# Optimization experiments

Hardware: AMD Instinct MI355X
Metric: run time of the kernel (lower is better)

The kernel has to match this reference:

```python
import jax, jax.numpy as jnp
import numpy as np

EPS = 1e-8


def setup_inputs() -> dict:
    key = jax.random.key(0)
    k1, k2 = jax.random.split(key)
    a = jax.random.normal(k1, (1, 256, 128, 128), dtype=jnp.float32)
    b = jax.random.normal(k2, (1, 256, 128, 128), dtype=jnp.float32)
    return {"a": a, "b": b}


def reference(a, b):
    # a: [n, c, h, w] rendered feats; b: [n, c, h2, w2] style feats (n == 1)
    n, c, h, w = a.shape
    a_flat = a.reshape(n, c, -1)            # [n, c, hw]
    b_flat = b.reshape(n, c, -1)            # [n, c, h2w2]

    # argmin_cos_distance: channel-wise L2 normalize, cosine distance, argmin
    b_norm = jnp.sqrt((b_flat * b_flat).sum(1, keepdims=True) + EPS)
    b_n = b_flat / (b_norm + EPS)
    a_norm = jnp.sqrt((a_flat * a_flat).sum(1, keepdims=True) + EPS)
    a_n = a_flat / (a_norm + EPS)
    d_mat = 1.0 - jnp.einsum('ncp,ncq->npq', a_n, b_n)   # [n, hw, h2w2]
    z_best = jnp.argmin(d_mat, axis=2)                    # [n, hw]

    # nn_feat_replace: gather matched (unnormalized) style features
    idx = jnp.broadcast_to(z_best[:, None, :], b_flat.shape)
    target = jnp.take_along_axis(b_flat, idx, axis=2).reshape(n, c, h, w)

    # cos_loss(a, target): cosine distance over channel dim, mean over pixels
    an = jnp.sqrt((a * a).sum(1, keepdims=True))
    tn = jnp.sqrt((target * target).sum(1, keepdims=True))
    cossim = ((a / (an + EPS)) * (target / (tn + EPS))).sum(1)  # [n, h, w]
    return (1.0 - cossim).mean()
```

## Files before the change

kernel.cpp:

```cpp
#include <hip/hip_runtime.h>
#include <hip/hip_fp8.h>
#include <stdint.h>

#define EPS 1e-8f

constexpr int C  = 256;
constexpr int HW = 16384;
constexpr int BM = 128;
constexpr int NG = 1024;

typedef __attribute__((ext_vector_type(4))) float floatx4;
typedef long long llong2 __attribute__((ext_vector_type(2)));
typedef unsigned char u8;
typedef unsigned int u32;
typedef unsigned long long u64;

__device__ inline u8 f2fp8(float x) {
    __hip_fp8_e4m3 h(x);
    return h.__x;
}

__device__ inline u32 pk4(float va, float vb, float vc, float vd) {
#if __has_builtin(__builtin_amdgcn_cvt_pk_fp8_f32)
    u32 w = __builtin_amdgcn_cvt_pk_fp8_f32(va, vb, 0, false);
    w = __builtin_amdgcn_cvt_pk_fp8_f32(vc, vd, w, true);
    return w;
#else
    return (u32)f2fp8(va) | ((u32)f2fp8(vb) << 8) |
           ((u32)f2fp8(vc) << 16) | ((u32)f2fp8(vd) << 24);
#endif
}

__global__ __launch_bounds__(256) void prep_kernel(const float* __restrict__ a,
                                                   const float* __restrict__ b,
                                                   float* __restrict__ sumsq_a,
                                                   float* __restrict__ sumsq_b,
                                                   u8* __restrict__ aF, u8* __restrict__ bF) {
    __shared__ float red[16][65];
    __shared__ float invb_sh[64];
    const int tid = threadIdx.x;
    const int pg = tid & 15, tc = tid >> 4;
    const int p0 = blockIdx.x * 64, pb = pg * 4;

    float4 bv[16];
    float ss0 = 0.f, ss1 = 0.f, ss2 = 0.f, ss3 = 0.f;
    #pragma unroll
    for (int i = 0; i < 16; ++i) {
        bv[i] = *(const float4*)&b[(size_t)(tc * 16 + i) * HW + p0 + pb];
        ss0 += bv[i].x * bv[i].x; ss1 += bv[i].y * bv[i].y;
        ss2 += bv[i].z * bv[i].z; ss3 += bv[i].w * bv[i].w;
    }
    red[tc][pb] = ss0; red[tc][pb + 1] = ss1; red[tc][pb + 2] = ss2; red[tc][pb + 3] = ss3;
    __syncthreads();
    if (tid < 64) {
        float B = 0.f;
        #pragma unroll
        for (int j = 0; j < 16; ++j) B += red[j][tid];
        sumsq_b[p0 + tid] = B;
        invb_sh[tid] = 1.0f / (sqrtf(B + EPS) + EPS);
    }
    __syncthreads();

    #pragma unroll
    for (int j = 0; j < 4; ++j) {
        int p = p0 + pb + j;
        float inv = invb_sh[pb + j];
        int g = p >> 4;
        #pragma unroll
        for (int h = 0; h < 2; ++h) {
            int cb = tc * 2 + h;
            float s0 = ((j == 0) ? bv[h*8+0].x : (j == 1) ? bv[h*8+0].y : (j == 2) ? bv[h*8+0].z : bv[h*8+0].w) * inv;
            float s1 = ((j == 0) ? bv[h*8+1].x : (j == 1) ? bv[h*8+1].y : (j == 2) ? bv[h*8+1].z : bv[h*8+1].w) * inv;
            float s2 = ((j == 0) ? bv[h*8+2].x : (j == 1) ? bv[h*8+2].y : (j == 2) ? bv[h*8+2].z : bv[h*8+2].w) * inv;
            float s3 = ((j == 0) ? bv[h*8+3].x : (j == 1) ? bv[h*8+3].y : (j == 2) ? bv[h*8+3].z : bv[h*8+3].w) * inv;
            float s4 = ((j == 0) ? bv[h*8+4].x : (j == 1) ? bv[h*8+4].y : (j == 2) ? bv[h*8+4].z : bv[h*8+4].w) * inv;
            float s5 = ((j == 0) ? bv[h*8+5].x : (j == 1) ? bv[h*8+5].y : (j == 2) ? bv[h*8+5].z : bv[h*8+5].w) * inv;
            float s6 = ((j == 0) ? bv[h*8+6].x : (j == 1) ? bv[h*8+6].y : (j == 2) ? bv[h*8+6].z : bv[h*8+6].w) * inv;
            float s7 = ((j == 0) ? bv[h*8+7].x : (j == 1) ? bv[h*8+7].y : (j == 2) ? bv[h*8+7].z : bv[h*8+7].w) * inv;
            u64 wv = (u64)pk4(s0, s1, s2, s3) | ((u64)pk4(s4, s5, s6, s7) << 32);
            int lane2 = (p & 15) + ((cb & 3) << 4);
            *(u64*)(bF + (((size_t)(g * 4 + (cb >> 3))) << 10) + lane2 * 16 + ((cb >> 2) & 1) * 8) = wv;
        }
    }

    float4 av[16];
    ss0 = ss1 = ss2 = ss3 = 0.f;
    #pragma unroll
    for (int i = 0; i < 16; ++i) {
        av[i] = *(const float4*)&a[(size_t)(tc * 16 + i) * HW + p0 + pb];
        ss0 += av[i].x * av[i].x; ss1 += av[i].y * av[i].y;
        ss2 += av[i].z * av[i].z; ss3 += av[i].w * av[i].w;
    }
    #pragma unroll
    for (int j = 0; j < 4; ++j) {
        int p = p0 + pb + j;
        int g = p >> 4;
        #pragma unroll
        for (int h = 0; h < 2; ++h) {
            int cb = tc * 2 + h;
            float s0 = (j == 0) ? av[h*8+0].x : (j == 1) ? av[h*8+0].y : (j == 2) ? av[h*8+0].z : av[h*8+0].w;
            float s1 = (j == 0) ? av[h*8+1].x : (j == 1) ? av[h*8+1].y : (j == 2) ? av[h*8+1].z : av[h*8+1].w;
            float s2 = (j == 0) ? av[h*8+2].x : (j == 1) ? av[h*8+2].y : (j == 2) ? av[h*8+2].z : av[h*8+2].w;
            float s3 = (j == 0) ? av[h*8+3].x : (j == 1) ? av[h*8+3].y : (j == 2) ? av[h*8+3].z : av[h*8+3].w;
            float s4 = (j == 0) ? av[h*8+4].x : (j == 1) ? av[h*8+4].y : (j == 2) ? av[h*8+4].z : av[h*8+4].w;
            float s5 = (j == 0) ? av[h*8+5].x : (j == 1) ? av[h*8+5].y : (j == 2) ? av[h*8+5].z : av[h*8+5].w;
            float s6 = (j == 0) ? av[h*8+6].x : (j == 1) ? av[h*8+6].y : (j == 2) ? av[h*8+6].z : av[h*8+6].w;
            float s7 = (j == 0) ? av[h*8+7].x : (j == 1) ? av[h*8+7].y : (j == 2) ? av[h*8+7].z : av[h*8+7].w;
            u64 wv = (u64)pk4(s0, s1, s2, s3) | ((u64)pk4(s4, s5, s6, s7) << 32);
            int lane2 = (p & 15) + ((cb & 3) << 4);
            *(u64*)(aF + (((size_t)(g * 4 + (cb >> 3))) << 10) + lane2 * 16 + ((cb >> 2) & 1) * 8) = wv;
        }
    }
    red[tc][pb] = ss0; red[tc][pb + 1] = ss1; red[tc][pb + 2] = ss2; red[tc][pb + 3] = ss3;
    __syncthreads();
    if (tid < 64) {
        float A = 0.f;
        #pragma unroll
        for (int j = 0; j < 16; ++j) A += red[j][tid];
        sumsq_a[p0 + tid] = A;
    }
}

__global__ __launch_bounds__(256, 3) void gemm_argmax(const u8* __restrict__ aF,
                                                      const u8* __restrict__ bF,
                                                      u64* __restrict__ packed) {
    const int tid = threadIdx.x;
    const int w = tid >> 6, lane = tid & 63;
    const int q4 = lane >> 4, r15 = lane & 15;
    const int wm = w >> 1, wn = w & 1;

    const u32 bid = blockIdx.x;
    const u32 ng = bid & 15;
    const u32 mt = bid >> 4;
    const int p0 = (int)mt * BM;

    const u8* gA = aF + ((size_t)(mt * 8 + wm * 4) * 4) * 1024 + (u32)lane * 16;
    llong2 Afr[4][4];
    #pragma unroll
    for (int mi = 0; mi < 4; ++mi)
        #pragma unroll
        for (int cp = 0; cp < 4; ++cp)
            Afr[mi][cp] = *(const llong2*)(gA + (u32)(mi * 4 + cp) * 1024);

    const u8* gB = bF + ((size_t)(ng * 64 + wn * 2)) * 4096 + (u32)lane * 16;

    float bestv[4][4];
    u32   bestq[4][4];
    #pragma unroll
    for (int mi = 0; mi < 4; ++mi)
        #pragma unroll
        for (int reg = 0; reg < 4; ++reg) { bestv[mi][reg] = -3.4e38f; bestq[mi][reg] = 0; }

    const u32 qlane = ng * 1024 + wn * 32 + (u32)r15;

    llong2 Bfr[2][2];
    #pragma unroll
    for (int ni = 0; ni < 2; ++ni)
        Bfr[0][ni] = *(const llong2*)(gB + (u32)ni * 4096u);

    for (int qt = 0; qt < 16; ++qt) {
        floatx4 acc[4][2] = {};
        #pragma unroll
        for (int cp = 0; cp < 4; ++cp) {
            const int cur = cp & 1, nxt = cur ^ 1;
            u32 nqt = (cp == 3) ? (u32)(qt + 1 < 16 ? qt + 1 : 15) : (u32)qt;
            u32 ncp = (cp == 3) ? 0u : (u32)(cp + 1);
            #pragma unroll
            for (int ni = 0; ni < 2; ++ni)
                Bfr[nxt][ni] = *(const llong2*)(gB + nqt * 16384u + (u32)ni * 4096u + ncp * 1024u);
            #pragma unroll
            for (int mi = 0; mi < 4; ++mi)
                #pragma unroll
                for (int ni = 0; ni < 2; ++ni)
                    acc[mi][ni] = __builtin_amdgcn_mfma_f32_16x16x32_fp8_fp8(
                        Afr[mi][cp].x, Bfr[cur][ni].x, acc[mi][ni], 0, 0, 0);
            #pragma unroll
            for (int mi = 0; mi < 4; ++mi)
                #pragma unroll
                for (int ni = 0; ni < 2; ++ni)
                    acc[mi][ni] = __builtin_amdgcn_mfma_f32_16x16x32_fp8_fp8(
                        Afr[mi][cp].y, Bfr[cur][ni].y, acc[mi][ni], 0, 0, 0);
        }
        #pragma unroll
        for (int mi = 0; mi < 4; ++mi)
            #pragma unroll
            for (int ni = 0; ni < 2; ++ni) {
                u32 qc = qlane + (u32)qt * 64 + (u32)ni * 16;
                #pragma unroll
                for (int reg = 0; reg < 4; ++reg) {
                    float v = acc[mi][ni][reg];
                    bool gt = v > bestv[mi][reg];
                    bestv[mi][reg] = gt ? v : bestv[mi][reg];
                    bestq[mi][reg] = gt ? qc : bestq[mi][reg];
                }
            }
    }

    #pragma unroll
    for (int mi = 0; mi < 4; ++mi)
        #pragma unroll
        for (int reg = 0; reg < 4; ++reg) {
            u32 m = __float_as_uint(bestv[mi][reg]);
            m = m ^ (u32)(((int)m >> 31) | 0x80000000u);
            u64 pk = ((u64)m << 32) | (u64)(0xFFFFFFFFu - bestq[mi][reg]);
            #pragma unroll
            for (int d = 1; d < 16; d <<= 1) {
                u64 o = __shfl_xor((unsigned long long)pk, d);
                pk = o > pk ? o : pk;
            }
            if (r15 == 0)
                atomicMax(&packed[p0 + wm * 64 + mi * 16 + q4 * 4 + reg], pk);
        }
}

__global__ void loss_kernel(const u64* __restrict__ packed,
                            const float* __restrict__ sumsq_a, const float* __restrict__ sumsq_b,
                            float* __restrict__ out) {
    int p = blockIdx.x * 256 + threadIdx.x;
    u64 pk = packed[p];
    u32 m = (u32)(pk >> 32);
    u32 u = (m & 0x80000000u) ? (m ^ 0x80000000u) : ~m;
    float s = __uint_as_float(u);
    u32 q = 0xFFFFFFFFu - (u32)(pk & 0xFFFFFFFFull);
    float A = sumsq_a[p], B = sumsq_b[q];
    float dot = s * (sqrtf(B + EPS) + EPS);
    float cossim = dot / ((sqrtf(A) + EPS) * (sqrtf(B) + EPS));
    float v = (1.0f - cossim) * (1.0f / (float)HW);
    #pragma unroll
    for (int d = 1; d < 64; d <<= 1) v += __shfl_xor(v, d);
    if ((threadIdx.x & 63) == 0) atomicAdd(out, v);
}

extern "C" void kernel_launch(void* const* d_in, const int* in_sizes, int n_in,
                              void* d_out, int out_size, void* d_ws, size_t ws_size,
                              hipStream_t stream) {
    const float* a = (const float*)d_in[0];
    const float* b = (const float*)d_in[1];
    float* out = (float*)d_out;
    char* ws = (char*)d_ws;

    u8*    aF      = (u8*)ws;
    u8*    bF      = (u8*)(ws + (size_t)4 * 1024 * 1024);
    float* sumsq_a = (float*)(ws + (size_t)8 * 1024 * 1024);
    float* sumsq_b = sumsq_a + HW;
    u64*   packed  = (u64*)(sumsq_b + HW);

    hipMemsetAsync(out, 0, sizeof(float), stream);
    hipMemsetAsync(packed, 0, (size_t)HW * sizeof(u64), stream);

    prep_kernel<<<dim3(HW / 64), 256, 0, stream>>>(a, b, sumsq_a, sumsq_b, aF, bF);
    gemm_argmax<<<dim3((HW / BM) * (HW / NG)), 256, 0, stream>>>(aF, bF, packed);
    loss_kernel<<<dim3(HW / 256), 256, 0, stream>>>(packed, sumsq_a, sumsq_b, out);
}
```

Before: 169.3 us.

## Pack argmax index into float low bits and re-tile prep kernel

The GEMM epilogue now biases the accumulators by 64 so every score is positive. It then ORs a 5-bit tile code into the low mantissa bits of each score and keeps a single unsigned max per output instead of a separate value and index pair. This cuts the compare/select work per MFMA tile roughly in half and frees registers. The cost is a slight loss of precision in the score and possibly different tie-breaking. Separately, the prep kernel is restructured to handle 16 pixels per block with 4 channels per thread, which gives more blocks and lower register pressure, at the cost of narrower 4-byte stores.

```diff
diff --git a/kernel.cpp b/kernel.cpp
--- a/kernel.cpp
+++ b/kernel.cpp
@@ -31,31 +31,38 @@
 #endif
 }
 
+__device__ inline float fc(const float4& f, int j) {
+    return j == 0 ? f.x : j == 1 ? f.y : j == 2 ? f.z : f.w;
+}
+
 __global__ __launch_bounds__(256) void prep_kernel(const float* __restrict__ a,
                                                    const float* __restrict__ b,
                                                    float* __restrict__ sumsq_a,
                                                    float* __restrict__ sumsq_b,
                                                    u8* __restrict__ aF, u8* __restrict__ bF) {
     __shared__ float red[16][65];
-    __shared__ float invb_sh[64];
+    __shared__ float invb_sh[16];
     const int tid = threadIdx.x;
-    const int pg = tid & 15, tc = tid >> 4;
-    const int p0 = blockIdx.x * 64, pb = pg * 4;
-
-    float4 bv[16];
+    const int pg = tid & 3, tc = tid >> 2;
+    const int p0 = blockIdx.x * 16, pb = pg * 4;
+    const int g = p0 >> 4;
+    const int cb = tc >> 1, cp = tc >> 4, half = (tc >> 3) & 1, qd = tc & 1;
+
+    float4 bv[4];
     float ss0 = 0.f, ss1 = 0.f, ss2 = 0.f, ss3 = 0.f;
     #pragma unroll
-    for (int i = 0; i < 16; ++i) {
-        bv[i] = *(const float4*)&b[(size_t)(tc * 16 + i) * HW + p0 + pb];
+    for (int i = 0; i < 4; ++i) {
+        bv[i] = *(const float4*)&b[(size_t)(tc * 4 + i) * HW + p0 + pb];
         ss0 += bv[i].x * bv[i].x; ss1 += bv[i].y * bv[i].y;
         ss2 += bv[i].z * bv[i].z; ss3 += bv[i].w * bv[i].w;
     }
-    red[tc][pb] = ss0; red[tc][pb + 1] = ss1; red[tc][pb + 2] = ss2; red[tc][pb + 3] = ss3;
-    __syncthreads();
-    if (tid < 64) {
+    red[pb + 0][tc] = ss0; red[pb + 1][tc] = ss1;
+    red[pb + 2][tc] = ss2; red[pb + 3][tc] = ss3;
+    __syncthreads();
+    if (tid < 16) {
         float B = 0.f;
         #pragma unroll
-        for (int j = 0; j < 16; ++j) B += red[j][tid];
+        for (int k = 0; k < 64; ++k) B += red[tid][k];
         sumsq_b[p0 + tid] = B;
         invb_sh[tid] = 1.0f / (sqrtf(B + EPS) + EPS);
     }
@@ -65,58 +72,35 @@
     for (int j = 0; j < 4; ++j) {
         int p = p0 + pb + j;
         float inv = invb_sh[pb + j];
-        int g = p >> 4;
-        #pragma unroll
-        for (int h = 0; h < 2; ++h) {
-            int cb = tc * 2 + h;
-            float s0 = ((j == 0) ? bv[h*8+0].x : (j == 1) ? bv[h*8+0].y : (j == 2) ? bv[h*8+0].z : bv[h*8+0].w) * inv;
-            float s1 = ((j == 0) ? bv[h*8+1].x : (j == 1) ? bv[h*8+1].y : (j == 2) ? bv[h*8+1].z : bv[h*8+1].w) * inv;
-            float s2 = ((j == 0) ? bv[h*8+2].x : (j == 1) ? bv[h*8+2].y : (j == 2) ? bv[h*8+2].z : bv[h*8+2].w) * inv;
-            float s3 = ((j == 0) ? bv[h*8+3].x : (j == 1) ? bv[h*8+3].y : (j == 2) ? bv[h*8+3].z : bv[h*8+3].w) * inv;
-            float s4 = ((j == 0) ? bv[h*8+4].x : (j == 1) ? bv[h*8+4].y : (j == 2) ? bv[h*8+4].z : bv[h*8+4].w) * inv;
-            float s5 = ((j == 0) ? bv[h*8+5].x : (j == 1) ? bv[h*8+5].y : (j == 2) ? bv[h*8+5].z : bv[h*8+5].w) * inv;
-            float s6 = ((j == 0) ? bv[h*8+6].x : (j == 1) ? bv[h*8+6].y : (j == 2) ? bv[h*8+6].z : bv[h*8+6].w) * inv;
-            float s7 = ((j == 0) ? bv[h*8+7].x : (j == 1) ? bv[h*8+7].y : (j == 2) ? bv[h*8+7].z : bv[h*8+7].w) * inv;
-            u64 wv = (u64)pk4(s0, s1, s2, s3) | ((u64)pk4(s4, s5, s6, s7) << 32);
-            int lane2 = (p & 15) + ((cb & 3) << 4);
-            *(u64*)(bF + (((size_t)(g * 4 + (cb >> 3))) << 10) + lane2 * 16 + ((cb >> 2) & 1) * 8) = wv;
-        }
-    }
-
-    float4 av[16];
+        u32 w = pk4(fc(bv[0], j) * inv, fc(bv[1], j) * inv,
+                    fc(bv[2], j) * inv, fc(bv[3], j) * inv);
+        int lane2 = (p & 15) + ((cb & 3) << 4);
+        *(u32*)(bF + (((size_t)(g * 4 + cp)) << 10) + lane2 * 16 + half * 8 + qd * 4) = w;
+    }
+
+    float4 av[4];
     ss0 = ss1 = ss2 = ss3 = 0.f;
     #pragma unroll
-    for (int i = 0; i < 16; ++i) {
-        av[i] = *(const float4*)&a[(size_t)(tc * 16 + i) * HW + p0 + pb];
+    for (int i = 0; i < 4; ++i) {
+        av[i] = *(const float4*)&a[(size_t)(tc * 4 + i) * HW + p0 + pb];
         ss0 += av[i].x * av[i].x; ss1 += av[i].y * av[i].y;
         ss2 += av[i].z * av[i].z; ss3 += av[i].w * av[i].w;
     }
     #pragma unroll
     for (int j = 0; j < 4; ++j) {
         int p = p0 + pb + j;
-        int g = p >> 4;
-        #pragma unroll
-        for (int h = 0; h < 2; ++h) {
-            int cb = tc * 2 + h;
-            float s0 = (j == 0) ? av[h*8+0].x : (j == 1) ? av[h*8+0].y : (j == 2) ? av[h*8+0].z : av[h*8+0].w;
-            float s1 = (j == 0) ? av[h*8+1].x : (j == 1) ? av[h*8+1].y : (j == 2) ? av[h*8+1].z : av[h*8+1].w;
-            float s2 = (j == 0) ? av[h*8+2].x : (j == 1) ? av[h*8+2].y : (j == 2) ? av[h*8+2].z : av[h*8+2].w;
-            float s3 = (j == 0) ? av[h*8+3].x : (j == 1) ? av[h*8+3].y : (j == 2) ? av[h*8+3].z : av[h*8+3].w;
-            float s4 = (j == 0) ? av[h*8+4].x : (j == 1) ? av[h*8+4].y : (j == 2) ? av[h*8+4].z : av[h*8+4].w;
-            float s5 = (j == 0) ? av[h*8+5].x : (j == 1) ? av[h*8+5].y : (j == 2) ? av[h*8+5].z : av[h*8+5].w;
-            float s6 = (j == 0) ? av[h*8+6].x : (j == 1) ? av[h*8+6].y : (j == 2) ? av[h*8+6].z : av[h*8+6].w;
-            float s7 = (j == 0) ? av[h*8+7].x : (j == 1) ? av[h*8+7].y : (j == 2) ? av[h*8+7].z : av[h*8+7].w;
-            u64 wv = (u64)pk4(s0, s1, s2, s3) | ((u64)pk4(s4, s5, s6, s7) << 32);
-            int lane2 = (p & 15) + ((cb & 3) << 4);
-            *(u64*)(aF + (((size_t)(g * 4 + (cb >> 3))) << 10) + lane2 * 16 + ((cb >> 2) & 1) * 8) = wv;
-        }
-    }
-    red[tc][pb] = ss0; red[tc][pb + 1] = ss1; red[tc][pb + 2] = ss2; red[tc][pb + 3] = ss3;
-    __syncthreads();
-    if (tid < 64) {
+        u32 w = pk4(fc(av[0], j), fc(av[1], j), fc(av[2], j), fc(av[3], j));
+        int lane2 = (p & 15) + ((cb & 3) << 4);
+        *(u32*)(aF + (((size_t)(g * 4 + cp)) << 10) + lane2 * 16 + half * 8 + qd * 4) = w;
+    }
+    __syncthreads();
+    red[pb + 0][tc] = ss0; red[pb + 1][tc] = ss1;
+    red[pb + 2][tc] = ss2; red[pb + 3][tc] = ss3;
+    __syncthreads();
+    if (tid < 16) {
         float A = 0.f;
         #pragma unroll
-        for (int j = 0; j < 16; ++j) A += red[j][tid];
+        for (int k = 0; k < 64; ++k) A += red[tid][k];
         sumsq_a[p0 + tid] = A;
     }
 }
@@ -134,6 +118,9 @@
     const u32 mt = bid >> 4;
     const int p0 = (int)mt * BM;
 
+    u32 maskv;
+    asm("v_mov_b32 %0, 0xFFFFFFE0" : "=v"(maskv));
+
     const u8* gA = aF + ((size_t)(mt * 8 + wm * 4) * 4) * 1024 + (u32)lane * 16;
     llong2 Afr[4][4];
     #pragma unroll
@@ -144,14 +131,10 @@
 
     const u8* gB = bF + ((size_t)(ng * 64 + wn * 2)) * 4096 + (u32)lane * 16;
 
-    float bestv[4][4];
-    u32   bestq[4][4];
-    #pragma unroll
-    for (int mi = 0; mi < 4; ++mi)
-        #pragma unroll
-        for (int reg = 0; reg < 4; ++reg) { bestv[mi][reg] = -3.4e38f; bestq[mi][reg] = 0; }
-
-    const u32 qlane = ng * 1024 + wn * 32 + (u32)r15;
+    u32 bestk[4][4] = {};
+    const u32 qbase = ng * 1024 + wn * 32 + (u32)r15;
+
+    const floatx4 BIAS = {64.0f, 64.0f, 64.0f, 64.0f};
 
     llong2 Bfr[2][2];
     #pragma unroll
@@ -159,7 +142,12 @@
         Bfr[0][ni] = *(const llong2*)(gB + (u32)ni * 4096u);
 
     for (int qt = 0; qt < 16; ++qt) {
-        floatx4 acc[4][2] = {};
+        floatx4 acc[4][2];
+        #pragma unroll
+        for (int mi = 0; mi < 4; ++mi)
+            #pragma unroll
+            for (int ni = 0; ni < 2; ++ni)
+                acc[mi][ni] = BIAS;
         #pragma unroll
         for (int cp = 0; cp < 4; ++cp) {
             const int cur = cp & 1, nxt = cur ^ 1;
@@ -182,27 +170,26 @@
                         Afr[mi][cp].y, Bfr[cur][ni].y, acc[mi][ni], 0, 0, 0);
         }
         #pragma unroll
-        for (int mi = 0; mi < 4; ++mi)
-            #pragma unroll
-            for (int ni = 0; ni < 2; ++ni) {
-                u32 qc = qlane + (u32)qt * 64 + (u32)ni * 16;
+        for (int ni = 0; ni < 2; ++ni) {
+            const u32 code = 31u - (u32)(qt * 2 + ni);
+            #pragma unroll
+            for (int mi = 0; mi < 4; ++mi)
                 #pragma unroll
                 for (int reg = 0; reg < 4; ++reg) {
-                    float v = acc[mi][ni][reg];
-                    bool gt = v > bestv[mi][reg];
-                    bestv[mi][reg] = gt ? v : bestv[mi][reg];
-                    bestq[mi][reg] = gt ? qc : bestq[mi][reg];
+                    u32 key = (__float_as_uint(acc[mi][ni][reg]) & maskv) | code;
+                    bestk[mi][reg] = bestk[mi][reg] > key ? bestk[mi][reg] : key;
                 }
-            }
+        }
     }
 
     #pragma unroll
     for (int mi = 0; mi < 4; ++mi)
         #pragma unroll
         for (int reg = 0; reg < 4; ++reg) {
-            u32 m = __float_as_uint(bestv[mi][reg]);
-            m = m ^ (u32)(((int)m >> 31) | 0x80000000u);
-            u64 pk = ((u64)m << 32) | (u64)(0xFFFFFFFFu - bestq[mi][reg]);
+            u32 k = bestk[mi][reg];
+            u32 code = 31u - (k & 31u);
+            u32 q = qbase + (code >> 1) * 64u + (code & 1u) * 16u;
+            u64 pk = ((u64)(k & 0xFFFFFFE0u) << 32) | (u64)(0xFFFFFFFFu - q);
             #pragma unroll
             for (int d = 1; d < 16; d <<= 1) {
                 u64 o = __shfl_xor((unsigned long long)pk, d);
@@ -218,9 +205,7 @@
                             float* __restrict__ out) {
     int p = blockIdx.x * 256 + threadIdx.x;
     u64 pk = packed[p];
-    u32 m = (u32)(pk >> 32);
-    u32 u = (m & 0x80000000u) ? (m ^ 0x80000000u) : ~m;
-    float s = __uint_as_float(u);
+    float s = __uint_as_float((u32)(pk >> 32)) - 64.0f;
     u32 q = 0xFFFFFFFFu - (u32)(pk & 0xFFFFFFFFull);
     float A = sumsq_a[p], B = sumsq_b[q];
     float dot = s * (sqrtf(B + EPS) + EPS);
@@ -248,7 +233,7 @@
     hipMemsetAsync(out, 0, sizeof(float), stream);
     hipMemsetAsync(packed, 0, (size_t)HW * sizeof(u64), stream);
 
-    prep_kernel<<<dim3(HW / 64), 256, 0, stream>>>(a, b, sumsq_a, sumsq_b, aF, bF);
+    prep_kernel<<<dim3(HW / 16), 256, 0, stream>>>(a, b, sumsq_a, sumsq_b, aF, bF);
     gemm_argmax<<<dim3((HW / BM) * (HW / NG)), 256, 0, stream>>>(aF, bF, packed);
     loss_kernel<<<dim3(HW / 256), 256, 0, stream>>>(packed, sumsq_a, sumsq_b, out);
 }
```

Measured after the change: 171.5 us. Within noise of the previous version (+1.3%).
